# Performance work log

Measured on AMD Instinct MI355X. Metric: run time of the kernel, lower is better.

Reference implementation:

```python
import jax, jax.numpy as jnp
import numpy as np

L = 2      # dec_num_layer
B = 32     # batch_size
T = 128    # block_len
H = 128    # dec_num_unit
F = 3      # code_rate_n / code_rate_k
D = 10


def _gru_cell(x, h, Wih, Whh, bih, bhh):
    # PyTorch GRU gate order: r, z, n
    gx = x @ Wih.T + bih
    gh = h @ Whh.T + bhh
    rx, zx, nx = jnp.split(gx, 3, axis=-1)
    rh, zh, nh = jnp.split(gh, 3, axis=-1)
    r = jax.nn.sigmoid(rx + rh)
    z = jax.nn.sigmoid(zx + zh)
    n = jnp.tanh(nx + r * nh)
    return (1.0 - z) * n + z * h


def _gru_stack(x, h, params):
    # x: [B, F], h: [L, B, H]; params: list of (Wih, Whh, bih, bhh) per layer
    hs = []
    inp = x
    for l, (Wih, Whh, bih, bhh) in enumerate(params):
        hl = _gru_cell(inp, h[l], Wih, Whh, bih, bhh)
        hs.append(hl)
        inp = hl
    return jnp.stack(hs), inp  # new hidden [L,B,H], top-layer output [B,H]


def _attend(h_raw, hist, i, attn_W, v_W, fc2_W, fc2_b):
    # h_raw: [L,B,H]; hist: [L,B,T,H]; growing-context attention with mask t<=i
    Ws, Wh = attn_W[:, :H], attn_W[:, H:]
    e = jnp.tanh((h_raw @ Ws.T)[:, :, None, :] + hist @ Wh.T)   # [L,B,T,H]
    logits = jnp.einsum('lbth,h->lbt', e, v_W[0])               # [L,B,T]
    mask = jnp.arange(T) <= i
    logits = jnp.where(mask[None, None, :], logits, -jnp.inf)
    a = jax.nn.softmax(logits, axis=-1)
    c = jnp.einsum('lbt,lbth->lbh', a, hist)                    # [L,B,H]
    return jnp.concatenate([c, h_raw], axis=-1) @ fc2_W.T + fc2_b


def _forward(received, params1, params2, attn_W, v_W, fc2_W, fc2_b, out_W, out_b):
    xs_seq = jnp.transpose(received, (1, 0, 2))  # [T,B,F]

    def step(carry, xs):
        h1, h2, hist1, hist2 = carry
        i, x = xs
        h1_raw, out1 = _gru_stack(x, h1, params1)
        h2_raw, out2 = _gru_stack(x, h2, params2)
        hist1 = hist1.at[:, :, i, :].set(h1_raw)
        hist2 = hist2.at[:, :, i, :].set(h2_raw)
        h1_att = _attend(h1_raw, hist1, i, attn_W, v_W, fc2_W, fc2_b)
        h2_att = _attend(h2_raw, hist2, i, attn_W, v_W, fc2_W, fc2_b)
        # torch skips the attention/fc2 update at step 0
        h1n = jnp.where(i > 0, h1_att, h1_raw)
        h2n = jnp.where(i > 0, h2_att, h2_raw)
        return (h1n, h2n, hist1, hist2), (out1, out2)

    z = jnp.zeros((L, B, H), dtype=received.dtype)
    zh = jnp.zeros((L, B, T, H), dtype=received.dtype)
    _, (o1, o2) = jax.lax.scan(step, (z, z, zh, zh), (jnp.arange(T), xs_seq))
    rnn1 = jnp.transpose(o1, (1, 0, 2))  # [B,T,H]
    rnn2 = jnp.transpose(o2, (1, 0, 2))

    idx = jnp.minimum(jnp.arange(T) + D, T - 1)
    rt_d = rnn2[:, idx, :]
    rnn_out = jnp.concatenate([rnn1, rt_d], axis=-1)            # [B,T,2H]
    dec = jnp.tanh(rnn_out @ out_W.T + out_b)                   # dec_act = tanh
    return jax.nn.sigmoid(dec)                                  # [B,T,1]


def setup_inputs() -> dict:
    key = jax.random.key(0)
    ks = iter(jax.random.split(key, 64))
    s = 0.05
    d = {"received": jax.random.normal(next(ks), (B, T, F), dtype=jnp.float32)}
    for dec in (1, 2):
        for l in range(L):
            inp = F if l == 0 else H
            d[f"Wih{dec}_{l}"] = jax.random.normal(next(ks), (3 * H, inp), dtype=jnp.float32) * s
            d[f"Whh{dec}_{l}"] = jax.random.normal(next(ks), (3 * H, H), dtype=jnp.float32) * s
            d[f"bih{dec}_{l}"] = jax.random.normal(next(ks), (3 * H,), dtype=jnp.float32) * s
            d[f"bhh{dec}_{l}"] = jax.random.normal(next(ks), (3 * H,), dtype=jnp.float32) * s
    d["attn_W"] = jax.random.normal(next(ks), (H, 2 * H), dtype=jnp.float32) * s
    d["v_W"] = jax.random.normal(next(ks), (1, H), dtype=jnp.float32) * s
    d["fc2_W"] = jax.random.normal(next(ks), (H, 2 * H), dtype=jnp.float32) * s
    d["fc2_b"] = jax.random.normal(next(ks), (H,), dtype=jnp.float32) * s
    d["out_W"] = jax.random.normal(next(ks), (1, 2 * H), dtype=jnp.float32) * s
    d["out_b"] = jax.random.normal(next(ks), (1,), dtype=jnp.float32) * s
    return d


def reference(received,
              Wih1_0, Whh1_0, bih1_0, bhh1_0, Wih1_1, Whh1_1, bih1_1, bhh1_1,
              Wih2_0, Whh2_0, bih2_0, bhh2_0, Wih2_1, Whh2_1, bih2_1, bhh2_1,
              attn_W, v_W, fc2_W, fc2_b, out_W, out_b):
    params1 = [(Wih1_0, Whh1_0, bih1_0, bhh1_0), (Wih1_1, Whh1_1, bih1_1, bhh1_1)]
    params2 = [(Wih2_0, Whh2_0, bih2_0, bhh2_0), (Wih2_1, Whh2_1, bih2_1, bhh2_1)]
    return _forward(received, params1, params2, attn_W, v_W, fc2_W, fc2_b, out_W, out_b)
```

## Files before the change

### kernel.cpp

```cpp
#include <hip/hip_runtime.h>

typedef _Float16 half_t;
typedef __attribute__((ext_vector_type(2))) _Float16 half2_t;

__device__ __forceinline__ half2_t bc2(unsigned int u){ return __builtin_bit_cast(half2_t, u); }
__device__ __forceinline__ float fdot2f(half2_t a, half2_t b, float c){
  return __builtin_amdgcn_fdot2(a, b, c, false);
}
__device__ __forceinline__ float rcp_f(float x){ return __builtin_amdgcn_rcpf(x); }
__device__ __forceinline__ float sigmoidf_(float x){ return rcp_f(1.0f+__expf(-x)); }
__device__ __forceinline__ float tanhf_(float x){ return 1.0f - 2.0f*rcp_f(__expf(2.0f*x)+1.0f); }

__device__ __forceinline__ float qxor1(float v){
  return __builtin_bit_cast(float, __builtin_amdgcn_mov_dpp(__builtin_bit_cast(int,v),0xB1,0xF,0xF,true));
}
__device__ __forceinline__ float qxor2(float v){
  return __builtin_bit_cast(float, __builtin_amdgcn_mov_dpp(__builtin_bit_cast(int,v),0x4E,0xF,0xF,true));
}
__device__ __forceinline__ float qsum4(float v){ v += qxor1(v); v += qxor2(v); return v; }

__device__ __forceinline__ void bar(){
  asm volatile("s_waitcnt lgkmcnt(0)\n\ts_barrier" ::: "memory");
}

__device__ __forceinline__ float dot32(const uint4* w, const uint4* x){
  float a=0.f,b=0.f,c=0.f,d=0.f;
  #pragma unroll
  for (int m=0;m<4;++m){
    a=fdot2f(bc2(w[m].x),bc2(x[m].x),a);
    b=fdot2f(bc2(w[m].y),bc2(x[m].y),b);
    c=fdot2f(bc2(w[m].z),bc2(x[m].z),c);
    d=fdot2f(bc2(w[m].w),bc2(x[m].w),d);
  }
  return (a+b)+(c+d);
}

template<int L>
__device__ __forceinline__ void phase6(int i, int tid,
    const half_t* shWh, const half_t* sWs0, const half_t* sWs1,
    const half_t* vw, float* probs0, float* probs1)
{
  const int sub = tid & (L-1);
  const int pid = tid / L;
  const int t6  = (L==2) ? (pid & 127) : (L==4) ? (pid & 63) : (pid & 31);
  const int l6  = (L==2) ? (pid >> 7)  : (L==4) ? (pid >> 6) : (pid >> 5);
  if (t6 <= i){
    const half_t* hwrow = shWh + (size_t)l6*(128*136) + t6*136;
    const half_t* swrow = l6 ? sWs1 : sWs0;
    const int M  = 16/L;
    const int m0 = M*sub;
    const int key = t6 & 15;
    float s = 0.f;
    #pragma unroll
    for (int mm=0; mm<M; ++mm){
      int m = m0+mm;
      uint4 hw = *reinterpret_cast<const uint4*>(hwrow + ((m^key)*8));
      uint4 sw = *reinterpret_cast<const uint4*>(swrow + 8*m);
      uint4 vv = *reinterpret_cast<const uint4*>(vw + 8*m);
      half2_t h2,s2,v2;
      h2=bc2(hw.x); s2=bc2(sw.x); v2=bc2(vv.x);
      s += tanhf_((float)s2[0]+(float)h2[0])*(float)v2[0];
      s += tanhf_((float)s2[1]+(float)h2[1])*(float)v2[1];
      h2=bc2(hw.y); s2=bc2(sw.y); v2=bc2(vv.y);
      s += tanhf_((float)s2[0]+(float)h2[0])*(float)v2[0];
      s += tanhf_((float)s2[1]+(float)h2[1])*(float)v2[1];
      h2=bc2(hw.z); s2=bc2(sw.z); v2=bc2(vv.z);
      s += tanhf_((float)s2[0]+(float)h2[0])*(float)v2[0];
      s += tanhf_((float)s2[1]+(float)h2[1])*(float)v2[1];
      h2=bc2(hw.w); s2=bc2(sw.w); v2=bc2(vv.w);
      s += tanhf_((float)s2[0]+(float)h2[0])*(float)v2[0];
      s += tanhf_((float)s2[1]+(float)h2[1])*(float)v2[1];
    }
    s += qxor1(s);
    if (L>=4) s += qxor2(s);
    if (L>=8) s += __shfl_xor(s,4);
    if (sub==0) (l6 ? probs1 : probs0)[t6] = __expf(s - 4.0f);
  }
}

__global__ void pack_k(const float* __restrict__ src, half_t* __restrict__ dst,
                       int R, int K, int ld, int coloff, int RT, int row_off){
  int idx = blockIdx.x*blockDim.x + threadIdx.x;
  if (idx >= R*K) return;
  int r = idx / K, k = idx - r*K;
  int kc = k >> 3, j = k & 7;
  dst[((size_t)kc*RT + row_off + r)*8 + j] = (half_t)src[(size_t)r*ld + coloff + k];
}

__launch_bounds__(512)
__global__ void gru_main(
    const float* __restrict__ received,
    const float* __restrict__ Wih0d0, const float* __restrict__ Wih0d1,
    const float* __restrict__ bx0d0, const float* __restrict__ bh0d0,
    const float* __restrict__ bx1d0, const float* __restrict__ bh1d0,
    const float* __restrict__ bx0d1, const float* __restrict__ bh0d1,
    const float* __restrict__ bx1d1, const float* __restrict__ bh1d1,
    const float* __restrict__ vW, const float* __restrict__ fc2b,
    const half_t* __restrict__ W0pack, const half_t* __restrict__ W1pack,
    const half_t* __restrict__ WsPack, const half_t* __restrict__ WhPack,
    const half_t* __restrict__ fc2Pack,
    half_t* __restrict__ o1h, half_t* __restrict__ o2h)
{
  const int dec = blockIdx.x >> 5;
  const int b   = blockIdx.x & 31;
  const int tid = threadIdx.x;
  const int q   = tid & 3;
  const int r   = tid >> 2;

  const float* bx0  = dec ? bx0d1 : bx0d0;
  const float* bh0  = dec ? bh0d1 : bh0d0;
  const float* bx1  = dec ? bx1d1 : bx1d0;
  const float* bh1  = dec ? bh1d1 : bh1d0;
  const float* Wih0 = dec ? Wih0d1 : Wih0d0;
  const half_t* W0  = W0pack + (size_t)dec*49152;
  const half_t* W1  = W1pack + (size_t)dec*98304;
  half_t* od = dec ? o2h : o1h;

  __shared__ __align__(16) half_t sh_hist[2][128*136];
  __shared__ __align__(16) half_t sh_histWh[2][128*136];
  __shared__ __align__(16) float  sh_gx[384];
  __shared__ __align__(16) float  sh_gh[384];
  __shared__ __align__(16) float  sh_g1x[384];
  __shared__ __align__(16) float  sh_g1h[384];
  __shared__ __align__(16) half_t sh_sWs16[2][128];
  __shared__ __align__(16) float  sh_probs[2][128];
  __shared__ __align__(16) float  sh_hatt32[2][128];
  __shared__ __align__(16) half_t sh_hatt_pk[2][128];
  __shared__ __align__(16) float  sh_hraw32[2][128];
  __shared__ __align__(16) half_t sh_hraw_pk[2][128];
  __shared__ __align__(16) half_t sh_fc2in[2][256];
  __shared__ __align__(16) half_t sh_vW16[128];
  __shared__ __align__(16) float4 sh_Wx4[384];

  float bA=0.f,bB=0.f,bC=0.f;
  if (q==0){ bA=bh0[r];     bB=bh1[r+128]; bC=bx1[r];     }
  else if (q==1){ bA=bh0[r+128]; bB=bh1[r+256]; bC=bx1[r+128]; }
  else if (q==2){ bA=bh0[r+256];                bC=bx1[r+256]; }
  else { bB=bh1[r]; }
  const float bF = fc2b[r];

  uint4 wP1[12];
  uint4 wP3[12];
  uint4 wP5[8];

  {
    uint4 z = make_uint4(0u,0u,0u,0u);
    uint4* ph = reinterpret_cast<uint4*>(&sh_hist[0][0]);
    uint4* pw = reinterpret_cast<uint4*>(&sh_histWh[0][0]);
    for (int j=tid; j<4352; j+=512){ ph[j]=z; pw[j]=z; }
  }
  if (tid < 256){ int l=tid>>7, rr=tid&127; sh_hatt32[l][rr]=0.f; sh_hatt_pk[l][rr]=(half_t)0.f; }
  if (tid < 128) sh_vW16[tid] = (half_t)vW[tid];
  if (tid < 384) sh_Wx4[tid] = make_float4(Wih0[tid*3], Wih0[tid*3+1], Wih0[tid*3+2], bx0[tid]);
  #pragma unroll
  for (int n=0;n<3;++n)
    #pragma unroll
    for (int m=0;m<4;++m)
      wP1[4*n+m] = *reinterpret_cast<const uint4*>(W0 + ((size_t)(4*q+m)*384 + r + 128*n)*8);
  bar();

  for (int i=0; i<128; ++i){
    {
      uint4 w1[12];
      #pragma unroll
      for (int n=0;n<3;++n)
        #pragma unroll
        for (int m=0;m<4;++m)
          w1[4*n+m] = *reinterpret_cast<const uint4*>(W1 + ((size_t)(4*q+m)*768 + 384 + r + 128*n)*8);
      uint4 xa[4];
      #pragma unroll
      for (int m=0;m<4;++m) xa[m] = *reinterpret_cast<const uint4*>(&sh_hatt_pk[0][32*q+8*m]);
      float a0 = dot32(&wP1[0],xa), a1 = dot32(&wP1[4],xa), a2 = dot32(&wP1[8],xa);
      uint4 xb[4];
      #pragma unroll
      for (int m=0;m<4;++m) xb[m] = *reinterpret_cast<const uint4*>(&sh_hatt_pk[1][32*q+8*m]);
      float a3 = dot32(&w1[0],xb), a4 = dot32(&w1[4],xb), a5 = dot32(&w1[8],xb);
      __builtin_amdgcn_sched_barrier(0);
      #pragma unroll
      for (int n=0;n<3;++n)
        #pragma unroll
        for (int m=0;m<4;++m)
          wP3[4*n+m] = *reinterpret_cast<const uint4*>(W1 + ((size_t)(4*q+m)*768 + r + 128*n)*8);
      a0=qsum4(a0); a1=qsum4(a1); a2=qsum4(a2);
      a3=qsum4(a3); a4=qsum4(a4); a5=qsum4(a5);
      if      (q==0){ sh_gh[r]      = a0+bA; sh_g1h[r+128] = a4+bB; }
      else if (q==1){ sh_gh[r+128]  = a1+bA; sh_g1h[r+256] = a5+bB; }
      else if (q==2){ sh_gh[r+256]  = a2+bA; }
      else          { sh_g1h[r]     = a3+bB; }
      if (tid < 384){
        const float* xr = &received[((size_t)b*128+i)*3];
        float4 wx = sh_Wx4[tid];
        sh_gx[tid] = wx.w + wx.x*xr[0] + wx.y*xr[1] + wx.z*xr[2];
      }
    }
    bar();
    if (tid < 128){
      float rr = sigmoidf_(sh_gx[tid]+sh_gh[tid]);
      float zz = sigmoidf_(sh_gx[128+tid]+sh_gh[128+tid]);
      float nn = tanhf_(sh_gx[256+tid] + rr*sh_gh[256+tid]);
      float h0 = (1.f-zz)*nn + zz*sh_hatt32[0][tid];
      sh_hraw32[0][tid]=h0;
      half_t hh=(half_t)h0;
      sh_hist[0][i*136 + ((tid>>3)^(i&15))*8 + (tid&7)] = hh;
      sh_hraw_pk[0][tid]=hh; sh_fc2in[0][128+tid]=hh;
    }
    bar();
    {
      uint4 xc[4];
      #pragma unroll
      for (int m=0;m<4;++m) xc[m] = *reinterpret_cast<const uint4*>(&sh_hraw_pk[0][32*q+8*m]);
      float a0 = dot32(&wP3[0],xc), a1 = dot32(&wP3[4],xc), a2 = dot32(&wP3[8],xc);
      __builtin_amdgcn_sched_barrier(0);
      #pragma unroll
      for (int m=0;m<4;++m){
        wP5[m]   = *reinterpret_cast<const uint4*>(WsPack + ((size_t)(4*q+m)*128 + r)*8);
        wP5[4+m] = *reinterpret_cast<const uint4*>(WhPack + ((size_t)(4*q+m)*128 + r)*8);
      }
      a0=qsum4(a0); a1=qsum4(a1); a2=qsum4(a2);
      if      (q==0) sh_g1x[r]     = a0+bC;
      else if (q==1) sh_g1x[r+128] = a1+bC;
      else if (q==2) sh_g1x[r+256] = a2+bC;
    }
    bar();
    if (tid < 128){
      float rr = sigmoidf_(sh_g1x[tid]+sh_g1h[tid]);
      float zz = sigmoidf_(sh_g1x[128+tid]+sh_g1h[128+tid]);
      float nn = tanhf_(sh_g1x[256+tid] + rr*sh_g1h[256+tid]);
      float h1 = (1.f-zz)*nn + zz*sh_hatt32[1][tid];
      sh_hraw32[1][tid]=h1;
      half_t hh=(half_t)h1;
      sh_hist[1][i*136 + ((tid>>3)^(i&15))*8 + (tid&7)] = hh;
      sh_hraw_pk[1][tid]=hh; sh_fc2in[1][128+tid]=hh;
      od[(size_t)(b*128+i)*128 + tid] = hh;
    }
    bar();
    {
      uint4 xa[4], xb[4];
      #pragma unroll
      for (int m=0;m<4;++m){
        xa[m] = *reinterpret_cast<const uint4*>(&sh_hraw_pk[0][32*q+8*m]);
        xb[m] = *reinterpret_cast<const uint4*>(&sh_hraw_pk[1][32*q+8*m]);
      }
      float sA0=qsum4(dot32(&wP5[0],xa));
      float sA1=qsum4(dot32(&wP5[0],xb));
      float sB0=qsum4(dot32(&wP5[4],xa));
      float sB1=qsum4(dot32(&wP5[4],xb));
      int phys = i*136 + ((r>>3)^(i&15))*8 + (r&7);
      if      (q==0) sh_sWs16[0][r] = (half_t)sA0;
      else if (q==1) sh_sWs16[1][r] = (half_t)sA1;
      else if (q==2) sh_histWh[0][phys] = (half_t)sB0;
      else           sh_histWh[1][phys] = (half_t)sB1;
    }
    bar();
    if (i > 0){
      if (i < 32)      phase6<8>(i, tid, &sh_histWh[0][0], &sh_sWs16[0][0], &sh_sWs16[1][0], &sh_vW16[0], &sh_probs[0][0], &sh_probs[1][0]);
      else if (i < 64) phase6<4>(i, tid, &sh_histWh[0][0], &sh_sWs16[0][0], &sh_sWs16[1][0], &sh_vW16[0], &sh_probs[0][0], &sh_probs[1][0]);
      else             phase6<2>(i, tid, &sh_histWh[0][0], &sh_sWs16[0][0], &sh_sWs16[1][0], &sh_vW16[0], &sh_probs[0][0], &sh_probs[1][0]);
      if (tid < 256){ int l=tid>>7, t=tid&127; if (t > i) sh_probs[l][t] = 0.f; }
      bar();
      uint4 wE[8];
      #pragma unroll
      for (int c=0;c<8;++c)
        wE[c] = *reinterpret_cast<const uint4*>(fc2Pack + ((size_t)(8*q+c)*128 + r)*8);
      {
        int ts=tid&15, oc=(tid>>4)&15, l8=tid>>8;
        float c0=0.f,c1=0.f,c2=0.f,c3=0.f,c4=0.f,c5=0.f,c6=0.f,c7=0.f, ps=0.f;
        int kmax = (i>>4)+1;
        for (int k=0;k<kmax;++k){
          int t = ts + 16*k;
          float p = sh_probs[l8][t];
          uint4 hv = *reinterpret_cast<const uint4*>(&sh_hist[l8][t*136 + ((oc^(t&15))*8)]);
          half2_t a=bc2(hv.x), e=bc2(hv.y), f=bc2(hv.z), g=bc2(hv.w);
          c0+=p*(float)a[0]; c1+=p*(float)a[1]; c2+=p*(float)e[0]; c3+=p*(float)e[1];
          c4+=p*(float)f[0]; c5+=p*(float)f[1]; c6+=p*(float)g[0]; c7+=p*(float)g[1];
          ps+=p;
        }
        c0+=qxor1(c0); c0+=qxor2(c0);  c1+=qxor1(c1); c1+=qxor2(c1);
        c2+=qxor1(c2); c2+=qxor2(c2);  c3+=qxor1(c3); c3+=qxor2(c3);
        c4+=qxor1(c4); c4+=qxor2(c4);  c5+=qxor1(c5); c5+=qxor2(c5);
        c6+=qxor1(c6); c6+=qxor2(c6);  c7+=qxor1(c7); c7+=qxor2(c7);
        ps+=qxor1(ps); ps+=qxor2(ps);
        c0+=__shfl_xor(c0,4); c1+=__shfl_xor(c1,4); c2+=__shfl_xor(c2,4); c3+=__shfl_xor(c3,4);
        c4+=__shfl_xor(c4,4); c5+=__shfl_xor(c5,4); c6+=__shfl_xor(c6,4); c7+=__shfl_xor(c7,4);
        ps+=__shfl_xor(ps,4);
        c0+=__shfl_xor(c0,8); c1+=__shfl_xor(c1,8); c2+=__shfl_xor(c2,8); c3+=__shfl_xor(c3,8);
        c4+=__shfl_xor(c4,8); c5+=__shfl_xor(c5,8); c6+=__shfl_xor(c6,8); c7+=__shfl_xor(c7,8);
        ps+=__shfl_xor(ps,8);
        if (ts==0){
          float inv = rcp_f(ps);
          half2_t o01={(half_t)(c0*inv),(half_t)(c1*inv)};
          half2_t o23={(half_t)(c2*inv),(half_t)(c3*inv)};
          half2_t o45={(half_t)(c4*inv),(half_t)(c5*inv)};
          half2_t o67={(half_t)(c6*inv),(half_t)(c7*inv)};
          *reinterpret_cast<uint4*>(&sh_fc2in[l8][oc*8]) =
              make_uint4((unsigned)__builtin_bit_cast(int,o01),(unsigned)__builtin_bit_cast(int,o23),
                         (unsigned)__builtin_bit_cast(int,o45),(unsigned)__builtin_bit_cast(int,o67));
        }
      }
      bar();
      {
        float e0=0.f, e1=0.f;
        #pragma unroll
        for (int h=0; h<2; ++h){
          uint4 x0[4], x1[4];
          #pragma unroll
          for (int m=0;m<4;++m){
            x0[m] = *reinterpret_cast<const uint4*>(&sh_fc2in[0][64*q + 32*h + 8*m]);
            x1[m] = *reinterpret_cast<const uint4*>(&sh_fc2in[1][64*q + 32*h + 8*m]);
          }
          e0 += dot32(&wE[4*h],x0);
          e1 += dot32(&wE[4*h],x1);
        }
        e0 = qsum4(e0); e1 = qsum4(e1);
        __builtin_amdgcn_sched_barrier(0);
        #pragma unroll
        for (int n=0;n<3;++n)
          #pragma unroll
          for (int m=0;m<4;++m)
            wP1[4*n+m] = *reinterpret_cast<const uint4*>(W0 + ((size_t)(4*q+m)*384 + r + 128*n)*8);
        if      (q==0){ float v=e0+bF; sh_hatt32[0][r]=v; sh_hatt_pk[0][r]=(half_t)v; }
        else if (q==1){ float v=e1+bF; sh_hatt32[1][r]=v; sh_hatt_pk[1][r]=(half_t)v; }
      }
    } else {
      #pragma unroll
      for (int n=0;n<3;++n)
        #pragma unroll
        for (int m=0;m<4;++m)
          wP1[4*n+m] = *reinterpret_cast<const uint4*>(W0 + ((size_t)(4*q+m)*384 + r + 128*n)*8);
      if (tid < 256){
        int l=tid>>7, row=tid&127;
        float hv = sh_hraw32[l][row];
        sh_hatt32[l][row]=hv; sh_hatt_pk[l][row]=(half_t)hv;
      }
    }
    bar();
  }
}

__global__ void out_kernel(const half_t* __restrict__ o1h, const half_t* __restrict__ o2h,
                           const float* __restrict__ outW, const float* __restrict__ outb,
                           float* __restrict__ dout){
  int tid = blockIdx.x*blockDim.x + threadIdx.x;
  int q = tid&3, job = tid>>2;
  int b = job>>7, t = job&127;
  int t2 = t+10; if (t2>127) t2=127;
  const half_t* r1 = o1h + (size_t)(b*128+t)*128;
  const half_t* r2 = o2h + (size_t)(b*128+t2)*128;
  float acc=0.f;
  for (int j=q*32; j<q*32+32; ++j) acc += outW[j]*(float)r1[j];
  for (int j=q*32; j<q*32+32; ++j) acc += outW[128+j]*(float)r2[j];
  acc += __shfl_xor(acc,1);
  acc += __shfl_xor(acc,2);
  if (q==0){
    float d = tanhf_(acc + outb[0]);
    dout[job] = rcp_f(1.f+__expf(-d));
  }
}

static inline void launch_pack(const void* src, half_t* dst, int R, int K, int ld,
                               int coloff, int RT, int row_off, hipStream_t s){
  int total = R*K;
  pack_k<<<(total+255)/256, 256, 0, s>>>((const float*)src, dst, R, K, ld, coloff, RT, row_off);
}

extern "C" void kernel_launch(void* const* d_in, const int* in_sizes, int n_in,
                              void* d_out, int out_size, void* d_ws, size_t ws_size,
                              hipStream_t stream) {
  const float* received = (const float*)d_in[0];
  const float* Wih1_0 = (const float*)d_in[1];
  const float* Whh1_0 = (const float*)d_in[2];
  const float* bih1_0 = (const float*)d_in[3];
  const float* bhh1_0 = (const float*)d_in[4];
  const float* Wih1_1 = (const float*)d_in[5];
  const float* Whh1_1 = (const float*)d_in[6];
  const float* bih1_1 = (const float*)d_in[7];
  const float* bhh1_1 = (const float*)d_in[8];
  const float* Wih2_0 = (const float*)d_in[9];
  const float* Whh2_0 = (const float*)d_in[10];
  const float* bih2_0 = (const float*)d_in[11];
  const float* bhh2_0 = (const float*)d_in[12];
  const float* Wih2_1 = (const float*)d_in[13];
  const float* Whh2_1 = (const float*)d_in[14];
  const float* bih2_1 = (const float*)d_in[15];
  const float* bhh2_1 = (const float*)d_in[16];
  const float* attn_W = (const float*)d_in[17];
  const float* v_W    = (const float*)d_in[18];
  const float* fc2_W  = (const float*)d_in[19];
  const float* fc2_b  = (const float*)d_in[20];
  const float* out_W  = (const float*)d_in[21];
  const float* out_b  = (const float*)d_in[22];

  half_t* ws = (half_t*)d_ws;
  half_t* W0pack  = ws + 0;
  half_t* W1pack  = ws + 98304;
  half_t* WsPack  = ws + 294912;
  half_t* WhPack  = ws + 311296;
  half_t* fc2Pack = ws + 327552;
  half_t* o1h     = ws + 360448;
  half_t* o2h     = ws + 884736;

  launch_pack(Whh1_0, W0pack,          384, 128, 128, 0, 384, 0, stream);
  launch_pack(Whh2_0, W0pack + 49152,  384, 128, 128, 0, 384, 0, stream);
  launch_pack(Wih1_1, W1pack,          384, 128, 128, 0, 768, 0, stream);
  launch_pack(Whh1_1, W1pack,          384, 128, 128, 0, 768, 384, stream);
  launch_pack(Wih2_1, W1pack + 98304,  384, 128, 128, 0, 768, 0, stream);
  launch_pack(Whh2_1, W1pack + 98304,  384, 128, 128, 0, 768, 384, stream);
  launch_pack(attn_W, WsPack,          128, 128, 256, 0,   128, 0, stream);
  launch_pack(attn_W, WhPack,          128, 128, 256, 128, 128, 0, stream);
  launch_pack(fc2_W,  fc2Pack,         128, 256, 256, 0,   128, 0, stream);

  gru_main<<<64, 512, 0, stream>>>(
      received,
      Wih1_0, Wih2_0,
      bih1_0, bhh1_0, bih1_1, bhh1_1,
      bih2_0, bhh2_0, bih2_1, bhh2_1,
      v_W, fc2_b,
      W0pack, W1pack, WsPack, WhPack, fc2Pack,
      o1h, o2h);

  out_kernel<<<64, 256, 0, stream>>>(o1h, o2h, out_W, out_b, (float*)d_out);
}
```

Measured before the change: 1.319 ms.

## Fuse GRU gate math into matvec phases to drop two barriers per step

Every lane of each quad now computes all three gate outputs for its row after the quad reduction, which is an all-lane reduction via DPP. The gate nonlinearities are then evaluated in registers right after the matvec instead of being written to shared memory and reread after a barrier. This removes the sh_gx/sh_gh/sh_g1x/sh_g1h shared buffers and two block-wide barriers per timestep on the serial recurrence path. In exchange, each quad lane redundantly computes the input projection and the gate transcendentals, and more bias values are held in registers.

```diff
diff --git a/kernel.cpp b/kernel.cpp
--- a/kernel.cpp
+++ b/kernel.cpp
@@ -118,10 +118,6 @@
 
   __shared__ __align__(16) half_t sh_hist[2][128*136];
   __shared__ __align__(16) half_t sh_histWh[2][128*136];
-  __shared__ __align__(16) float  sh_gx[384];
-  __shared__ __align__(16) float  sh_gh[384];
-  __shared__ __align__(16) float  sh_g1x[384];
-  __shared__ __align__(16) float  sh_g1h[384];
   __shared__ __align__(16) half_t sh_sWs16[2][128];
   __shared__ __align__(16) float  sh_probs[2][128];
   __shared__ __align__(16) float  sh_hatt32[2][128];
@@ -132,11 +128,9 @@
   __shared__ __align__(16) half_t sh_vW16[128];
   __shared__ __align__(16) float4 sh_Wx4[384];
 
-  float bA=0.f,bB=0.f,bC=0.f;
-  if (q==0){ bA=bh0[r];     bB=bh1[r+128]; bC=bx1[r];     }
-  else if (q==1){ bA=bh0[r+128]; bB=bh1[r+256]; bC=bx1[r+128]; }
-  else if (q==2){ bA=bh0[r+256];                bC=bx1[r+256]; }
-  else { bB=bh1[r]; }
+  const float bA0=bh0[r], bA1=bh0[r+128], bA2=bh0[r+256];
+  const float bB0=bh1[r], bB1=bh1[r+128], bB2=bh1[r+256];
+  const float bC0=bx1[r], bC1=bx1[r+128], bC2=bx1[r+256];
   const float bF = fc2b[r];
 
   uint4 wP1[12];
@@ -159,7 +153,10 @@
       wP1[4*n+m] = *reinterpret_cast<const uint4*>(W0 + ((size_t)(4*q+m)*384 + r + 128*n)*8);
   bar();
 
+  float g1h0=0.f, g1h1=0.f, g1h2=0.f;
+
   for (int i=0; i<128; ++i){
+    const int phys = i*136 + ((r>>3)^(i&15))*8 + (r&7);
     {
       uint4 w1[12];
       #pragma unroll
@@ -181,57 +178,49 @@
         #pragma unroll
         for (int m=0;m<4;++m)
           wP3[4*n+m] = *reinterpret_cast<const uint4*>(W1 + ((size_t)(4*q+m)*768 + r + 128*n)*8);
-      a0=qsum4(a0); a1=qsum4(a1); a2=qsum4(a2);
-      a3=qsum4(a3); a4=qsum4(a4); a5=qsum4(a5);
-      if      (q==0){ sh_gh[r]      = a0+bA; sh_g1h[r+128] = a4+bB; }
-      else if (q==1){ sh_gh[r+128]  = a1+bA; sh_g1h[r+256] = a5+bB; }
-      else if (q==2){ sh_gh[r+256]  = a2+bA; }
-      else          { sh_g1h[r]     = a3+bB; }
-      if (tid < 384){
-        const float* xr = &received[((size_t)b*128+i)*3];
-        float4 wx = sh_Wx4[tid];
-        sh_gx[tid] = wx.w + wx.x*xr[0] + wx.y*xr[1] + wx.z*xr[2];
-      }
-    }
-    bar();
-    if (tid < 128){
-      float rr = sigmoidf_(sh_gx[tid]+sh_gh[tid]);
-      float zz = sigmoidf_(sh_gx[128+tid]+sh_gh[128+tid]);
-      float nn = tanhf_(sh_gx[256+tid] + rr*sh_gh[256+tid]);
-      float h0 = (1.f-zz)*nn + zz*sh_hatt32[0][tid];
-      sh_hraw32[0][tid]=h0;
-      half_t hh=(half_t)h0;
-      sh_hist[0][i*136 + ((tid>>3)^(i&15))*8 + (tid&7)] = hh;
-      sh_hraw_pk[0][tid]=hh; sh_fc2in[0][128+tid]=hh;
+      a0=qsum4(a0)+bA0; a1=qsum4(a1)+bA1; a2=qsum4(a2)+bA2;
+      g1h0=qsum4(a3)+bB0; g1h1=qsum4(a4)+bB1; g1h2=qsum4(a5)+bB2;
+      const float* xr = &received[((size_t)b*128+i)*3];
+      float xv0=xr[0], xv1=xr[1], xv2=xr[2];
+      float4 wxa=sh_Wx4[r], wxb=sh_Wx4[r+128], wxc=sh_Wx4[r+256];
+      float gxr = wxa.w + wxa.x*xv0 + wxa.y*xv1 + wxa.z*xv2;
+      float gxz = wxb.w + wxb.x*xv0 + wxb.y*xv1 + wxb.z*xv2;
+      float gxn = wxc.w + wxc.x*xv0 + wxc.y*xv1 + wxc.z*xv2;
+      float rr = sigmoidf_(gxr + a0);
+      float zz = sigmoidf_(gxz + a1);
+      float nn = tanhf_(gxn + rr*a2);
+      float h0 = (1.f-zz)*nn + zz*sh_hatt32[0][r];
+      if (q==0){
+        sh_hraw32[0][r]=h0;
+        half_t hh=(half_t)h0;
+        sh_hist[0][phys]=hh;
+        sh_hraw_pk[0][r]=hh; sh_fc2in[0][128+r]=hh;
+      }
     }
     bar();
     {
       uint4 xc[4];
       #pragma unroll
       for (int m=0;m<4;++m) xc[m] = *reinterpret_cast<const uint4*>(&sh_hraw_pk[0][32*q+8*m]);
-      float a0 = dot32(&wP3[0],xc), a1 = dot32(&wP3[4],xc), a2 = dot32(&wP3[8],xc);
+      float c0 = dot32(&wP3[0],xc), c1 = dot32(&wP3[4],xc), c2 = dot32(&wP3[8],xc);
       __builtin_amdgcn_sched_barrier(0);
       #pragma unroll
       for (int m=0;m<4;++m){
         wP5[m]   = *reinterpret_cast<const uint4*>(WsPack + ((size_t)(4*q+m)*128 + r)*8);
         wP5[4+m] = *reinterpret_cast<const uint4*>(WhPack + ((size_t)(4*q+m)*128 + r)*8);
       }
-      a0=qsum4(a0); a1=qsum4(a1); a2=qsum4(a2);
-      if      (q==0) sh_g1x[r]     = a0+bC;
-      else if (q==1) sh_g1x[r+128] = a1+bC;
-      else if (q==2) sh_g1x[r+256] = a2+bC;
-    }
-    bar();
-    if (tid < 128){
-      float rr = sigmoidf_(sh_g1x[tid]+sh_g1h[tid]);
-      float zz = sigmoidf_(sh_g1x[128+tid]+sh_g1h[128+tid]);
-      float nn = tanhf_(sh_g1x[256+tid] + rr*sh_g1h[256+tid]);
-      float h1 = (1.f-zz)*nn + zz*sh_hatt32[1][tid];
-      sh_hraw32[1][tid]=h1;
-      half_t hh=(half_t)h1;
-      sh_hist[1][i*136 + ((tid>>3)^(i&15))*8 + (tid&7)] = hh;
-      sh_hraw_pk[1][tid]=hh; sh_fc2in[1][128+tid]=hh;
-      od[(size_t)(b*128+i)*128 + tid] = hh;
+      c0=qsum4(c0)+bC0; c1=qsum4(c1)+bC1; c2=qsum4(c2)+bC2;
+      float rr = sigmoidf_(c0 + g1h0);
+      float zz = sigmoidf_(c1 + g1h1);
+      float nn = tanhf_(c2 + rr*g1h2);
+      float h1 = (1.f-zz)*nn + zz*sh_hatt32[1][r];
+      if (q==0){
+        sh_hraw32[1][r]=h1;
+        half_t hh=(half_t)h1;
+        sh_hist[1][phys]=hh;
+        sh_hraw_pk[1][r]=hh; sh_fc2in[1][128+r]=hh;
+        od[(size_t)(b*128+i)*128 + r]=hh;
+      }
     }
     bar();
     {
@@ -245,7 +234,6 @@
       float sA1=qsum4(dot32(&wP5[0],xb));
       float sB0=qsum4(dot32(&wP5[4],xa));
       float sB1=qsum4(dot32(&wP5[4],xb));
-      int phys = i*136 + ((r>>3)^(i&15))*8 + (r&7);
       if      (q==0) sh_sWs16[0][r] = (half_t)sA0;
       else if (q==1) sh_sWs16[1][r] = (half_t)sA1;
       else if (q==2) sh_histWh[0][phys] = (half_t)sB0;
```

Result: no change. 1.300 ms (-1.5%).
